# Performance work log

Hardware: AMD Instinct MI355X
Metric: run time of the kernel (lower is better)

The kernel has to match this reference:

```python
import jax, jax.numpy as jnp
import numpy as np

N = 100000      # nodes
E = 1600000     # edges
F_IN = 512      # num_features
H = 128         # hidden
C = 40          # num_classes
K = 10          # Chebyshev order


def setup_inputs() -> dict:
    key = jax.random.key(0)
    ks = jax.random.split(key, 6)
    x = jax.random.normal(ks[0], (N, F_IN), dtype=jnp.float32)
    edge_index = jax.random.randint(ks[1], (2, E), 0, N, dtype=jnp.int32)
    W1 = jax.random.normal(ks[2], (F_IN, H), dtype=jnp.float32) / np.sqrt(F_IN).astype(np.float32)
    b1 = jnp.zeros((H,), dtype=jnp.float32)
    W2 = jax.random.normal(ks[3], (H, C), dtype=jnp.float32) / np.sqrt(H).astype(np.float32)
    b2 = jnp.zeros((C,), dtype=jnp.float32)
    # Chebyshev coefficients temp[K+1]
    temp = 1.0 + 0.1 * jax.random.normal(ks[4], (K + 1,), dtype=jnp.float32)
    return {"x": x, "edge_index": edge_index, "W1": W1, "b1": b1, "W2": W2, "b2": b2, "temp": temp}


def reference(x, edge_index, W1, b1, W2, b2, temp):
    # MLP encoder (eval mode: dropout is identity)
    h = jax.nn.relu(x @ W1 + b1)          # [N, H]
    h = h @ W2 + b2                        # [N, C]

    # gcn_norm: add self-loops, symmetric normalization
    self_loop = jnp.arange(N, dtype=edge_index.dtype)
    row = jnp.concatenate([edge_index[0], self_loop])   # [E+N]
    col = jnp.concatenate([edge_index[1], self_loop])
    deg = jax.ops.segment_sum(jnp.ones_like(row, dtype=jnp.float32), row, num_segments=N)
    dis = jnp.where(deg > 0, jax.lax.rsqrt(jnp.maximum(deg, 1.0)), 0.0)
    norm = dis[row] * dis[col]             # [E+N]

    def prop(v):  # A_hat @ v : gather-scale-scatter over edges
        return jax.ops.segment_sum(norm[:, None] * v[col], row, num_segments=N)

    # Chebyshev recurrence: Tx_k = 2*A_hat*Tx_{k-1} - Tx_{k-2}
    Tx0 = h
    Tx1 = prop(h)
    out0 = temp[0] * Tx0 + temp[1] * Tx1

    def body(carry, coe):
        t0, t1, acc = carry
        t2 = 2.0 * prop(t1) - t0
        return (t1, t2, acc + coe * t2), None

    (_, _, out), _ = jax.lax.scan(body, (Tx0, Tx1, out0), temp[2:])
    return jax.nn.log_softmax(out, axis=1)
```

## Files before the change

### kernel.cpp

```cpp
#include <hip/hip_runtime.h>
#include <hip/hip_bf16.h>
#include <cstdint>
#include <cstddef>

#define NN   100000
#define EE   1600000
#define FIN  512
#define HID  128
#define CC   40
#define KORD 10
#define SHB  80
#define SHSTRIDE ((size_t)NN * SHB)

typedef __attribute__((ext_vector_type(4))) float f4;
typedef __attribute__((ext_vector_type(8))) short short8_t;
typedef __attribute__((ext_vector_type(4))) unsigned int u4;

__device__ __forceinline__ unsigned short cvt_bf16(float f) {
  union { float f; unsigned u; } a; a.f = f;
  unsigned r = a.u + 0x7fffu + ((a.u >> 16) & 1u);
  return (unsigned short)(r >> 16);
}
__device__ __forceinline__ unsigned pk_bf(float a, float b) {
  union { float f; unsigned u; } x, y; x.f = a; y.f = b;
  unsigned ra = x.u + 0x7fffu + ((x.u >> 16) & 1u);
  unsigned rb = y.u + 0x7fffu + ((y.u >> 16) & 1u);
  return (ra >> 16) | (rb & 0xffff0000u);
}
__device__ __forceinline__ unsigned pk_tr(float a, float b) {
  union { float f; unsigned u; } x, y; x.f = a; y.f = b;
  return (x.u >> 16) | (y.u & 0xffff0000u);
}
__device__ __forceinline__ f4 cvf2(unsigned lo, unsigned hi) {
  union { unsigned u; float f; } a, b, c, d;
  a.u = lo << 16; b.u = lo & 0xffff0000u;
  c.u = hi << 16; d.u = hi & 0xffff0000u;
  f4 r; r.x = a.f; r.y = b.f; r.z = c.f; r.w = d.f; return r;
}

__global__ __launch_bounds__(256) void k_dw(const int* __restrict__ rowI, int* __restrict__ deg,
                                            const float* __restrict__ W1, unsigned short* __restrict__ W1T,
                                            int ndeg) {
  int b = blockIdx.x;
  if (b < ndeg) {
    int i = b * 256 + threadIdx.x;
    if (i < EE) atomicAdd(&deg[rowI[i]], 1);
  } else {
    int idx = (b - ndeg) * 256 + threadIdx.x;
    int k = idx >> 7, n = idx & 127;
    W1T[(k >> 5) * 4096 + n * 32 + (k & 31)] = cvt_bf16(W1[idx]);
  }
}

__global__ __launch_bounds__(256) void k_scan1(const int* __restrict__ cnt, int* __restrict__ excl,
                                               int* __restrict__ bsums) {
  __shared__ int s[256];
  int tid = threadIdx.x;
  int base = blockIdx.x * 1024 + tid * 4;
  int v0 = (base + 0 < NN) ? cnt[base + 0] + 1 : 0;
  int v1 = (base + 1 < NN) ? cnt[base + 1] + 1 : 0;
  int v2 = (base + 2 < NN) ? cnt[base + 2] + 1 : 0;
  int v3 = (base + 3 < NN) ? cnt[base + 3] + 1 : 0;
  int tsum = v0 + v1 + v2 + v3;
  s[tid] = tsum;
  __syncthreads();
  for (int off = 1; off < 256; off <<= 1) {
    int t = (tid >= off) ? s[tid - off] : 0;
    __syncthreads();
    if (tid >= off) s[tid] += t;
    __syncthreads();
  }
  int run = s[tid] - tsum;
  if (tid == 255) bsums[blockIdx.x] = s[255];
  if (base + 0 < NN) excl[base + 0] = run; run += v0;
  if (base + 1 < NN) excl[base + 1] = run; run += v1;
  if (base + 2 < NN) excl[base + 2] = run; run += v2;
  if (base + 3 < NN) excl[base + 3] = run;
}

__global__ __launch_bounds__(128) void k_scan2(int* __restrict__ bsums, int nb) {
  __shared__ int s[128];
  int tid = threadIdx.x;
  int v = (tid < nb) ? bsums[tid] : 0;
  s[tid] = v;
  __syncthreads();
  for (int off = 1; off < 128; off <<= 1) {
    int t = (tid >= off) ? s[tid - off] : 0;
    __syncthreads();
    if (tid >= off) s[tid] += t;
    __syncthreads();
  }
  if (tid < nb) bsums[tid] = s[tid] - v;
}

__global__ __launch_bounds__(256) void k_scan3(const int* __restrict__ cnt, int* __restrict__ rs,
                                               int* __restrict__ cur, const int* __restrict__ bsums,
                                               float* __restrict__ dis, float* __restrict__ sqd,
                                               float* __restrict__ invd) {
  int i = blockIdx.x * 256 + threadIdx.x;
  if (i < NN) {
    int v = rs[i] + bsums[i >> 10];
    rs[i] = v;
    cur[i] = v;
    int d = cnt[i] + 1;
    if (i == NN - 1) rs[NN] = v + d;
    float fd = (float)d;
    dis[i]  = rsqrtf(fd);
    sqd[i]  = sqrtf(fd);
    invd[i] = 1.0f / fd;
  }
}

#define SLICE_ROWS (NN / 8)
#define SC_CHUNK   2048
__global__ __launch_bounds__(256) void k_scatter(const int* __restrict__ rowI, const int* __restrict__ colI,
                                                 int* __restrict__ cur, int* __restrict__ colS) {
  int slice = blockIdx.x & 7;
  int chunk = blockIdx.x >> 3;
  int lo = slice * SLICE_ROWS, hi = lo + SLICE_ROWS;
#pragma unroll
  for (int t = 0; t < SC_CHUNK / 256; ++t) {
    int i = chunk * SC_CHUNK + t * 256 + threadIdx.x;
    if (i < EE + NN) {
      int r = (i < EE) ? rowI[i] : (i - EE);
      if (r >= lo && r < hi) {
        int c = (i < EE) ? colI[i] : r;
        int pos = atomicAdd(&cur[r], 1);
        colS[pos] = c * SHB;
      }
    }
  }
}

#define LDK 40
__global__ __launch_bounds__(256) void k_gemm1(const float* __restrict__ x, const unsigned short* __restrict__ W1T,
                                               const float* __restrict__ b1, float* __restrict__ h1) {
  __shared__ __align__(16) float As_f[128 * 32];
  __shared__ __align__(16) short Bs_s[128][LDK];
  int tid  = threadIdx.x;
  int wave = tid >> 6, lane = tid & 63;
  int blockRow = blockIdx.x * 128;
  int wr = (wave & 1) * 64, wc = (wave >> 1) * 64;
  int l15 = lane & 15, hi4 = lane >> 4;

  int sr = (wave << 5) + (lane >> 3);
  int sslot = lane & 7;

  f4 acc[4][4] = {};

  for (int k0 = 0; k0 < FIN; k0 += 32) {
#pragma unroll
    for (int c = 0; c < 4; ++c) {
      int row = sr + c * 8;
      int gr = blockRow + row;
      int lslot = sslot ^ (row & 7);
      const float* gp = x + (size_t)gr * FIN + k0 + lslot * 4;
      float* lp = &As_f[(wave << 10) + (c << 8)];
      if (gr < NN) {
        __builtin_amdgcn_global_load_lds(
            (const __attribute__((address_space(1))) unsigned int*)gp,
            (__attribute__((address_space(3))) unsigned int*)lp, 16, 0, 0);
      }
    }

    const unsigned short* Wt = W1T + (k0 >> 5) * 4096;
    short8_t q0 = *(const short8_t*)&Wt[tid * 16];
    short8_t q1 = *(const short8_t*)&Wt[tid * 16 + 8];
    int bn = tid >> 1, bkk = (tid & 1) * 16;
    *(short8_t*)&Bs_s[bn][bkk]     = q0;
    *(short8_t*)&Bs_s[bn][bkk + 8] = q1;

    __syncthreads();

    short8_t afr[4], bfr[4];
#pragma unroll
    for (int m = 0; m < 4; ++m) {
      int row = wr + m * 16 + l15;
      int s0 = (hi4 * 2) ^ (row & 7);
      int s1 = (hi4 * 2 + 1) ^ (row & 7);
      f4 a0 = *(const f4*)&As_f[(row << 5) + s0 * 4];
      f4 a1 = *(const f4*)&As_f[(row << 5) + s1 * 4];
      u4 p;
      p.x = pk_tr(a0.x, a0.y); p.y = pk_tr(a0.z, a0.w);
      p.z = pk_tr(a1.x, a1.y); p.w = pk_tr(a1.z, a1.w);
      afr[m] = *(short8_t*)&p;
    }
#pragma unroll
    for (int n = 0; n < 4; ++n) bfr[n] = *(const short8_t*)&Bs_s[wc + n * 16 + l15][hi4 * 8];
#pragma unroll
    for (int m = 0; m < 4; ++m)
#pragma unroll
      for (int n = 0; n < 4; ++n)
        acc[m][n] = __builtin_amdgcn_mfma_f32_16x16x32_bf16(afr[m], bfr[n], acc[m][n], 0, 0, 0);

    __syncthreads();
  }

  float bias[4];
#pragma unroll
  for (int n = 0; n < 4; ++n) bias[n] = b1[wc + n * 16 + l15];
#pragma unroll
  for (int m = 0; m < 4; ++m) {
    int baseRow = blockRow + wr + m * 16 + hi4 * 4;
#pragma unroll
    for (int n = 0; n < 4; ++n) {
      int col = wc + n * 16 + l15;
#pragma unroll
      for (int r = 0; r < 4; ++r) {
        int grow = baseRow + r;
        if (grow < NN) h1[(size_t)grow * HID + col] = fmaxf(acc[m][n][r] + bias[n], 0.f);
      }
    }
  }
}

__global__ __launch_bounds__(256) void k_gemm2(const float* __restrict__ h1, const float* __restrict__ W2,
                                               const float* __restrict__ b2, const float* __restrict__ temp,
                                               const float* __restrict__ dis,
                                               unsigned short* __restrict__ sh0) {
  __shared__ float sW[HID * CC];
  __shared__ float sb[CC];
  int tid = threadIdx.x;
  for (int i = tid; i < HID * CC; i += 256) sW[i] = W2[i];
  if (tid < CC) sb[tid] = b2[tid];
  __syncthreads();
  int gid = blockIdx.x * 256 + tid;
  if (gid >= NN * 20) return;
  int row = gid / 20;
  int c2  = (gid - row * 20) * 2;
  const float* hr = h1 + (size_t)row * HID;
  float a0 = sb[c2], a1 = sb[c2 + 1];
#pragma unroll 8
  for (int k = 0; k < HID; ++k) {
    float hv = hr[k];
    a0 = fmaf(hv, sW[k * CC + c2], a0);
    a1 = fmaf(hv, sW[k * CC + c2 + 1], a1);
  }
  float dv = dis[row];
  *(unsigned*)((char*)sh0 + (size_t)row * SHB + c2 * 2) = pk_bf(a0 * dv, a1 * dv);
}

template <int MODE>
__global__ __launch_bounds__(256) void k_prop(const unsigned short* __restrict__ shIn,
                                              const unsigned short* __restrict__ shPrev,
                                              unsigned short* __restrict__ shOut,
                                              const int* __restrict__ colS,
                                              const int* __restrict__ rs,
                                              const float* __restrict__ invd) {
  int lane = threadIdx.x & 63;
  int wave = threadIdx.x >> 6;
  int grp  = lane / 5;
  int fi   = lane - grp * 5;
  int node = blockIdx.x * 48 + wave * 12 + grp;
  bool active = (grp < 12) && (node < NN);
  int s = 0, e = 0;
  if (active) { s = rs[node]; e = rs[node + 1]; }
  const char* base = (const char*)shIn + fi * 16;
  f4 lo0 = {0.f,0.f,0.f,0.f}, hi0 = lo0, lo1 = lo0, hi1 = lo0;
  f4 lo2 = lo0, hi2 = lo0, lo3 = lo0, hi3 = lo0;
  int j = s;
  for (; j + 8 <= e; j += 8) {
    int c0 = colS[j],     c1 = colS[j + 1], c2 = colS[j + 2], c3 = colS[j + 3];
    int c4 = colS[j + 4], c5 = colS[j + 5], c6 = colS[j + 6], c7 = colS[j + 7];
    u4 p0 = *(const u4*)(base + c0);
    u4 p1 = *(const u4*)(base + c1);
    u4 p2 = *(const u4*)(base + c2);
    u4 p3 = *(const u4*)(base + c3);
    u4 p4 = *(const u4*)(base + c4);
    u4 p5 = *(const u4*)(base + c5);
    u4 p6 = *(const u4*)(base + c6);
    u4 p7 = *(const u4*)(base + c7);
    lo0 += cvf2(p0.x, p0.y); hi0 += cvf2(p0.z, p0.w);
    lo1 += cvf2(p1.x, p1.y); hi1 += cvf2(p1.z, p1.w);
    lo2 += cvf2(p2.x, p2.y); hi2 += cvf2(p2.z, p2.w);
    lo3 += cvf2(p3.x, p3.y); hi3 += cvf2(p3.z, p3.w);
    lo0 += cvf2(p4.x, p4.y); hi0 += cvf2(p4.z, p4.w);
    lo1 += cvf2(p5.x, p5.y); hi1 += cvf2(p5.z, p5.w);
    lo2 += cvf2(p6.x, p6.y); hi2 += cvf2(p6.z, p6.w);
    lo3 += cvf2(p7.x, p7.y); hi3 += cvf2(p7.z, p7.w);
  }
  if (j + 4 <= e) {
    int c0 = colS[j], c1 = colS[j + 1], c2 = colS[j + 2], c3 = colS[j + 3];
    u4 p0 = *(const u4*)(base + c0);
    u4 p1 = *(const u4*)(base + c1);
    u4 p2 = *(const u4*)(base + c2);
    u4 p3 = *(const u4*)(base + c3);
    lo0 += cvf2(p0.x, p0.y); hi0 += cvf2(p0.z, p0.w);
    lo1 += cvf2(p1.x, p1.y); hi1 += cvf2(p1.z, p1.w);
    lo2 += cvf2(p2.x, p2.y); hi2 += cvf2(p2.z, p2.w);
    lo3 += cvf2(p3.x, p3.y); hi3 += cvf2(p3.z, p3.w);
    j += 4;
  }
  if (j + 2 <= e) {
    u4 p0 = *(const u4*)(base + colS[j]);
    u4 p1 = *(const u4*)(base + colS[j + 1]);
    lo0 += cvf2(p0.x, p0.y); hi0 += cvf2(p0.z, p0.w);
    lo1 += cvf2(p1.x, p1.y); hi1 += cvf2(p1.z, p1.w);
    j += 2;
  }
  if (j < e) {
    u4 p0 = *(const u4*)(base + colS[j]);
    lo2 += cvf2(p0.x, p0.y); hi2 += cvf2(p0.z, p0.w);
  }

  if (active) {
    f4 slo = (lo0 + lo1) + (lo2 + lo3);
    f4 shi = (hi0 + hi1) + (hi2 + hi3);
    float iv = invd[node];
    size_t ro = (size_t)node * SHB + fi * 16;
    f4 wlo, whi;
    if (MODE == 0) {
      wlo = iv * slo; whi = iv * shi;
    } else {
      u4 pp = *(const u4*)((const char*)shPrev + ro);
      f4 plo = cvf2(pp.x, pp.y), phi = cvf2(pp.z, pp.w);
      wlo = (2.f * iv) * slo - plo;
      whi = (2.f * iv) * shi - phi;
    }
    u4 pk;
    pk.x = pk_bf(wlo.x, wlo.y); pk.y = pk_bf(wlo.z, wlo.w);
    pk.z = pk_bf(whi.x, whi.y); pk.w = pk_bf(whi.z, whi.w);
    *(u4*)((char*)shOut + ro) = pk;
  }
}

__global__ __launch_bounds__(256) void k_comb(const unsigned short* __restrict__ shBase,
                                              float* __restrict__ outF,
                                              const float* __restrict__ sqd,
                                              const float* __restrict__ temp) {
  int lane = threadIdx.x & 63;
  int wave = threadIdx.x >> 6;
  int grp  = lane / 5;
  int fi   = lane - grp * 5;
  int node = blockIdx.x * 48 + wave * 12 + grp;
  if (grp >= 12 || node >= NN) return;

  const char* p = (const char*)shBase + (size_t)node * SHB + fi * 16;
  f4 alo = {0.f,0.f,0.f,0.f}, ahi = alo;
#pragma unroll
  for (int k = 0; k <= KORD; ++k) {
    u4 pp = *(const u4*)(p + (size_t)k * SHSTRIDE);
    float tk = temp[k];
    alo += tk * cvf2(pp.x, pp.y);
    ahi += tk * cvf2(pp.z, pp.w);
  }
  float sq = sqd[node];
  alo *= sq; ahi *= sq;

  int gb = grp * 5;
  float m = fmaxf(fmaxf(fmaxf(alo.x, alo.y), fmaxf(alo.z, alo.w)),
                  fmaxf(fmaxf(ahi.x, ahi.y), fmaxf(ahi.z, ahi.w)));
  float mm = m;
#pragma unroll
  for (int j = 0; j < 5; ++j) mm = fmaxf(mm, __shfl(m, gb + j));
  float ss = expf(alo.x - mm) + expf(alo.y - mm) + expf(alo.z - mm) + expf(alo.w - mm)
           + expf(ahi.x - mm) + expf(ahi.y - mm) + expf(ahi.z - mm) + expf(ahi.w - mm);
  float tot = 0.f;
#pragma unroll
  for (int j = 0; j < 5; ++j) tot += __shfl(ss, gb + j);
  float lse = mm + logf(tot);
  alo -= lse; ahi -= lse;
  size_t o = (size_t)node * CC + fi * 8;
  *(f4*)&outF[o]     = alo;
  *(f4*)&outF[o + 4] = ahi;
}

extern "C" void kernel_launch(void* const* d_in, const int* in_sizes, int n_in,
                              void* d_out, int out_size, void* d_ws, size_t ws_size,
                              hipStream_t stream) {
  const float* x    = (const float*)d_in[0];
  const int*   ei   = (const int*)d_in[1];
  const float* W1   = (const float*)d_in[2];
  const float* b1   = (const float*)d_in[3];
  const float* W2   = (const float*)d_in[4];
  const float* b2   = (const float*)d_in[5];
  const float* temp = (const float*)d_in[6];
  const int* rowI = ei;
  const int* colI = ei + EE;
  float* out = (float*)d_out;

  char* w = (char*)d_ws;
  auto alloc = [&](size_t bytes) -> void* {
    void* p = (void*)w;
    w += (bytes + 255) & ~(size_t)255;
    return p;
  };
  int*   deg   = (int*)  alloc((size_t)NN * 4);
  float* dis   = (float*)alloc((size_t)NN * 4);
  float* sqd   = (float*)alloc((size_t)NN * 4);
  float* invd  = (float*)alloc((size_t)NN * 4);
  int*   rs    = (int*)  alloc((size_t)(NN + 1) * 4);
  int*   cur   = (int*)  alloc((size_t)NN * 4);
  int*   bsums = (int*)  alloc(512 * 4);
  unsigned short* W1T = (unsigned short*)alloc((size_t)FIN * HID * 2);
  unsigned short* shAll = (unsigned short*)alloc(SHSTRIDE * (KORD + 1));
  int*   colS  = (int*)  alloc((size_t)(EE + NN) * 4);
  float* h1    = (float*)alloc((size_t)NN * HID * 4);

  auto sh = [&](int k) -> unsigned short* {
    return (unsigned short*)((char*)shAll + (size_t)k * SHSTRIDE);
  };

  hipMemsetAsync(deg, 0, (size_t)NN * 4, stream);

  const int NDEG = (EE + 255) / 256;
  const int NW1T = FIN * HID / 256;
  k_dw<<<NDEG + NW1T, 256, 0, stream>>>(rowI, deg, W1, W1T, NDEG);

  int nb = (NN + 1023) / 1024;
  k_scan1<<<nb, 256, 0, stream>>>(deg, rs, bsums);
  k_scan2<<<1, 128, 0, stream>>>(bsums, nb);
  k_scan3<<<(NN + 255) / 256, 256, 0, stream>>>(deg, rs, cur, bsums, dis, sqd, invd);

  const int NCH = (EE + NN + SC_CHUNK - 1) / SC_CHUNK;
  k_scatter<<<8 * NCH, 256, 0, stream>>>(rowI, colI, cur, colS);

  k_gemm1<<<(NN + 127) / 128, 256, 0, stream>>>(x, W1T, b1, h1);
  k_gemm2<<<(NN * 20 + 255) / 256, 256, 0, stream>>>(h1, W2, b2, temp, dis, sh(0));

  int G = (NN + 47) / 48;
  k_prop<0><<<G, 256, 0, stream>>>(sh(0), sh(0), sh(1), colS, rs, invd);
  for (int k = 2; k <= KORD; ++k) {
    k_prop<1><<<G, 256, 0, stream>>>(sh(k - 1), sh(k - 2), sh(k), colS, rs, invd);
  }

  k_comb<<<G, 256, 0, stream>>>(shAll, out, sqd, temp);
}
```

Baseline: 625.8 us.

## Split feature layout into column blocks and propagate block-wise with XCC-aware chunk scheduling

Each Chebyshev term is stored as three separate column blocks (features 0-15, 16-31, 32-39) instead of 80-byte interleaved rows. Each propagation kernel processes one block per workgroup, and workgroups claim chunks through atomic cursors whose starting block depends on the XCC ID. The aim is to shrink the gathered working set per pass so it fits in the per-XCC L2 cache, and to use vectorized colS loads. In exchange it adds atomic work distribution, more index loads per edge (colS is read once per block pass), and a dependence on the hardware XCC register.

```diff
diff --git a/kernel.cpp b/kernel.cpp
--- a/kernel.cpp
+++ b/kernel.cpp
@@ -9,12 +9,18 @@
 #define HID  128
 #define CC   40
 #define KORD 10
-#define SHB  80
-#define SHSTRIDE ((size_t)NN * SHB)
+#define SHSTRIDE ((size_t)NN * 80)
+#define BLKB ((size_t)NN * 32)
+#define BLKC ((size_t)NN * 64)
+#define CHA 782
+#define CHB 782
+#define CHC 391
+#define PGRID 2048
 
 typedef __attribute__((ext_vector_type(4))) float f4;
 typedef __attribute__((ext_vector_type(8))) short short8_t;
 typedef __attribute__((ext_vector_type(4))) unsigned int u4;
+typedef __attribute__((ext_vector_type(4), aligned(4))) int i4u;
 
 __device__ __forceinline__ unsigned short cvt_bf16(float f) {
   union { float f; unsigned u; } a; a.f = f;
@@ -126,7 +132,7 @@
       if (r >= lo && r < hi) {
         int c = (i < EE) ? colI[i] : r;
         int pos = atomicAdd(&cur[r], 1);
-        colS[pos] = c * SHB;
+        colS[pos] = c * 32;
       }
     }
   }
@@ -212,6 +218,12 @@
       }
     }
   }
+}
+
+__device__ __forceinline__ size_t sh_off(int node, int fi) {
+  return (fi < 2) ? ((size_t)node * 32 + fi * 16)
+       : (fi < 4) ? (BLKB + (size_t)node * 32 + (fi - 2) * 16)
+                  : (BLKC + (size_t)node * 16);
 }
 
 __global__ __launch_bounds__(256) void k_gemm2(const float* __restrict__ h1, const float* __restrict__ W2,
@@ -237,90 +249,182 @@
     a1 = fmaf(hv, sW[k * CC + c2 + 1], a1);
   }
   float dv = dis[row];
-  *(unsigned*)((char*)sh0 + (size_t)row * SHB + c2 * 2) = pk_bf(a0 * dv, a1 * dv);
+  size_t ro;
+  if (c2 < 16)      ro = (size_t)row * 32 + c2 * 2;
+  else if (c2 < 32) ro = BLKB + (size_t)row * 32 + (c2 - 16) * 2;
+  else              ro = BLKC + (size_t)row * 16 + (c2 - 32) * 2;
+  *(unsigned*)((char*)sh0 + ro) = pk_bf(a0 * dv, a1 * dv);
 }
 
 template <int MODE>
-__global__ __launch_bounds__(256) void k_prop(const unsigned short* __restrict__ shIn,
-                                              const unsigned short* __restrict__ shPrev,
-                                              unsigned short* __restrict__ shOut,
-                                              const int* __restrict__ colS,
-                                              const int* __restrict__ rs,
-                                              const float* __restrict__ invd) {
-  int lane = threadIdx.x & 63;
-  int wave = threadIdx.x >> 6;
-  int grp  = lane / 5;
-  int fi   = lane - grp * 5;
-  int node = blockIdx.x * 48 + wave * 12 + grp;
-  bool active = (grp < 12) && (node < NN);
-  int s = 0, e = 0;
-  if (active) { s = rs[node]; e = rs[node + 1]; }
-  const char* base = (const char*)shIn + fi * 16;
-  f4 lo0 = {0.f,0.f,0.f,0.f}, hi0 = lo0, lo1 = lo0, hi1 = lo0;
-  f4 lo2 = lo0, hi2 = lo0, lo3 = lo0, hi3 = lo0;
-  int j = s;
-  for (; j + 8 <= e; j += 8) {
-    int c0 = colS[j],     c1 = colS[j + 1], c2 = colS[j + 2], c3 = colS[j + 3];
-    int c4 = colS[j + 4], c5 = colS[j + 5], c6 = colS[j + 6], c7 = colS[j + 7];
-    u4 p0 = *(const u4*)(base + c0);
-    u4 p1 = *(const u4*)(base + c1);
-    u4 p2 = *(const u4*)(base + c2);
-    u4 p3 = *(const u4*)(base + c3);
-    u4 p4 = *(const u4*)(base + c4);
-    u4 p5 = *(const u4*)(base + c5);
-    u4 p6 = *(const u4*)(base + c6);
-    u4 p7 = *(const u4*)(base + c7);
-    lo0 += cvf2(p0.x, p0.y); hi0 += cvf2(p0.z, p0.w);
-    lo1 += cvf2(p1.x, p1.y); hi1 += cvf2(p1.z, p1.w);
-    lo2 += cvf2(p2.x, p2.y); hi2 += cvf2(p2.z, p2.w);
-    lo3 += cvf2(p3.x, p3.y); hi3 += cvf2(p3.z, p3.w);
-    lo0 += cvf2(p4.x, p4.y); hi0 += cvf2(p4.z, p4.w);
-    lo1 += cvf2(p5.x, p5.y); hi1 += cvf2(p5.z, p5.w);
-    lo2 += cvf2(p6.x, p6.y); hi2 += cvf2(p6.z, p6.w);
-    lo3 += cvf2(p7.x, p7.y); hi3 += cvf2(p7.z, p7.w);
-  }
-  if (j + 4 <= e) {
-    int c0 = colS[j], c1 = colS[j + 1], c2 = colS[j + 2], c3 = colS[j + 3];
-    u4 p0 = *(const u4*)(base + c0);
-    u4 p1 = *(const u4*)(base + c1);
-    u4 p2 = *(const u4*)(base + c2);
-    u4 p3 = *(const u4*)(base + c3);
-    lo0 += cvf2(p0.x, p0.y); hi0 += cvf2(p0.z, p0.w);
-    lo1 += cvf2(p1.x, p1.y); hi1 += cvf2(p1.z, p1.w);
-    lo2 += cvf2(p2.x, p2.y); hi2 += cvf2(p2.z, p2.w);
-    lo3 += cvf2(p3.x, p3.y); hi3 += cvf2(p3.z, p3.w);
-    j += 4;
-  }
-  if (j + 2 <= e) {
-    u4 p0 = *(const u4*)(base + colS[j]);
-    u4 p1 = *(const u4*)(base + colS[j + 1]);
-    lo0 += cvf2(p0.x, p0.y); hi0 += cvf2(p0.z, p0.w);
-    lo1 += cvf2(p1.x, p1.y); hi1 += cvf2(p1.z, p1.w);
-    j += 2;
-  }
-  if (j < e) {
-    u4 p0 = *(const u4*)(base + colS[j]);
-    lo2 += cvf2(p0.x, p0.y); hi2 += cvf2(p0.z, p0.w);
-  }
-
-  if (active) {
-    f4 slo = (lo0 + lo1) + (lo2 + lo3);
-    f4 shi = (hi0 + hi1) + (hi2 + hi3);
-    float iv = invd[node];
-    size_t ro = (size_t)node * SHB + fi * 16;
-    f4 wlo, whi;
-    if (MODE == 0) {
-      wlo = iv * slo; whi = iv * shi;
-    } else {
-      u4 pp = *(const u4*)((const char*)shPrev + ro);
-      f4 plo = cvf2(pp.x, pp.y), phi = cvf2(pp.z, pp.w);
-      wlo = (2.f * iv) * slo - plo;
-      whi = (2.f * iv) * shi - phi;
-    }
-    u4 pk;
-    pk.x = pk_bf(wlo.x, wlo.y); pk.y = pk_bf(wlo.z, wlo.w);
-    pk.z = pk_bf(whi.x, whi.y); pk.w = pk_bf(whi.z, whi.w);
-    *(u4*)((char*)shOut + ro) = pk;
+__global__ __launch_bounds__(256) void k_prop3(const unsigned short* __restrict__ shIn,
+                                               const unsigned short* __restrict__ shPrev,
+                                               unsigned short* __restrict__ shOut,
+                                               const int* __restrict__ colS,
+                                               const int* __restrict__ rs,
+                                               const float* __restrict__ invd,
+                                               int* __restrict__ cursors) {
+  __shared__ int s_pass, s_chunk;
+  if (threadIdx.x == 0) {
+    unsigned xcc;
+    asm volatile("s_getreg_b32 %0, hwreg(HW_REG_XCC_ID, 0, 32)" : "=s"(xcc));
+    int x = (int)(xcc & 7);
+    int pref = (x < 3) ? 0 : (x < 6) ? 1 : 2;
+    int pass = -1, chunk = -1;
+    for (int t = 0; t < 3; ++t) {
+      int p = pref + t; if (p >= 3) p -= 3;
+      int lim = (p == 0) ? CHA : (p == 1) ? CHB : CHC;
+      int c = atomicAdd(&cursors[p], 1);
+      if (c < lim) { pass = p; chunk = c; break; }
+    }
+    s_pass = pass; s_chunk = chunk;
+  }
+  __syncthreads();
+  int pass = s_pass;
+  if (pass < 0) return;
+  int chunk = s_chunk;
+  int lane = threadIdx.x & 63, wave = threadIdx.x >> 6;
+
+  if (pass < 2) {
+    size_t pb = (pass == 0) ? (size_t)0 : BLKB;
+    int grp = lane >> 1, fi = lane & 1;
+    int node = chunk * 128 + wave * 32 + grp;
+    bool act = node < NN;
+    int s = 0, e = 0;
+    if (act) { s = rs[node]; e = rs[node + 1]; }
+    const char* base = (const char*)shIn + pb + fi * 16;
+    f4 a0 = {0.f,0.f,0.f,0.f}, b0 = a0, a1 = a0, b1 = a0;
+    int j = s;
+    for (; j + 8 <= e; j += 8) {
+      i4u ca = *(const i4u*)&colS[j];
+      i4u cb = *(const i4u*)&colS[j + 4];
+      u4 p0 = *(const u4*)(base + ca.x);
+      u4 p1 = *(const u4*)(base + ca.y);
+      u4 p2 = *(const u4*)(base + ca.z);
+      u4 p3 = *(const u4*)(base + ca.w);
+      u4 p4 = *(const u4*)(base + cb.x);
+      u4 p5 = *(const u4*)(base + cb.y);
+      u4 p6 = *(const u4*)(base + cb.z);
+      u4 p7 = *(const u4*)(base + cb.w);
+      a0 += cvf2(p0.x, p0.y); b0 += cvf2(p0.z, p0.w);
+      a1 += cvf2(p1.x, p1.y); b1 += cvf2(p1.z, p1.w);
+      a0 += cvf2(p2.x, p2.y); b0 += cvf2(p2.z, p2.w);
+      a1 += cvf2(p3.x, p3.y); b1 += cvf2(p3.z, p3.w);
+      a0 += cvf2(p4.x, p4.y); b0 += cvf2(p4.z, p4.w);
+      a1 += cvf2(p5.x, p5.y); b1 += cvf2(p5.z, p5.w);
+      a0 += cvf2(p6.x, p6.y); b0 += cvf2(p6.z, p6.w);
+      a1 += cvf2(p7.x, p7.y); b1 += cvf2(p7.z, p7.w);
+    }
+    if (j + 4 <= e) {
+      i4u ca = *(const i4u*)&colS[j];
+      u4 p0 = *(const u4*)(base + ca.x);
+      u4 p1 = *(const u4*)(base + ca.y);
+      u4 p2 = *(const u4*)(base + ca.z);
+      u4 p3 = *(const u4*)(base + ca.w);
+      a0 += cvf2(p0.x, p0.y); b0 += cvf2(p0.z, p0.w);
+      a1 += cvf2(p1.x, p1.y); b1 += cvf2(p1.z, p1.w);
+      a0 += cvf2(p2.x, p2.y); b0 += cvf2(p2.z, p2.w);
+      a1 += cvf2(p3.x, p3.y); b1 += cvf2(p3.z, p3.w);
+      j += 4;
+    }
+    if (j + 2 <= e) {
+      u4 p0 = *(const u4*)(base + colS[j]);
+      u4 p1 = *(const u4*)(base + colS[j + 1]);
+      a0 += cvf2(p0.x, p0.y); b0 += cvf2(p0.z, p0.w);
+      a1 += cvf2(p1.x, p1.y); b1 += cvf2(p1.z, p1.w);
+      j += 2;
+    }
+    if (j < e) {
+      u4 p0 = *(const u4*)(base + colS[j]);
+      a0 += cvf2(p0.x, p0.y); b0 += cvf2(p0.z, p0.w);
+    }
+    if (act) {
+      f4 slo = a0 + a1, shi = b0 + b1;
+      float iv = invd[node];
+      size_t ro = pb + (size_t)node * 32 + fi * 16;
+      f4 wlo, whi;
+      if (MODE == 0) {
+        wlo = iv * slo; whi = iv * shi;
+      } else {
+        u4 pp = __builtin_nontemporal_load((const u4*)((const char*)shPrev + ro));
+        f4 plo = cvf2(pp.x, pp.y), phi = cvf2(pp.z, pp.w);
+        wlo = (2.f * iv) * slo - plo;
+        whi = (2.f * iv) * shi - phi;
+      }
+      u4 pk;
+      pk.x = pk_bf(wlo.x, wlo.y); pk.y = pk_bf(wlo.z, wlo.w);
+      pk.z = pk_bf(whi.x, whi.y); pk.w = pk_bf(whi.z, whi.w);
+      *(u4*)((char*)shOut + ro) = pk;
+    }
+  } else {
+    int node = chunk * 256 + wave * 64 + lane;
+    bool act = node < NN;
+    int s = 0, e = 0;
+    if (act) { s = rs[node]; e = rs[node + 1]; }
+    const char* base = (const char*)shIn + BLKC;
+    f4 a0 = {0.f,0.f,0.f,0.f}, b0 = a0, a1 = a0, b1 = a0;
+    int j = s;
+    for (; j + 8 <= e; j += 8) {
+      i4u ca = *(const i4u*)&colS[j];
+      i4u cb = *(const i4u*)&colS[j + 4];
+      u4 p0 = *(const u4*)(base + (ca.x >> 1));
+      u4 p1 = *(const u4*)(base + (ca.y >> 1));
+      u4 p2 = *(const u4*)(base + (ca.z >> 1));
+      u4 p3 = *(const u4*)(base + (ca.w >> 1));
+      u4 p4 = *(const u4*)(base + (cb.x >> 1));
+      u4 p5 = *(const u4*)(base + (cb.y >> 1));
+      u4 p6 = *(const u4*)(base + (cb.z >> 1));
+      u4 p7 = *(const u4*)(base + (cb.w >> 1));
+      a0 += cvf2(p0.x, p0.y); b0 += cvf2(p0.z, p0.w);
+      a1 += cvf2(p1.x, p1.y); b1 += cvf2(p1.z, p1.w);
+      a0 += cvf2(p2.x, p2.y); b0 += cvf2(p2.z, p2.w);
+      a1 += cvf2(p3.x, p3.y); b1 += cvf2(p3.z, p3.w);
+      a0 += cvf2(p4.x, p4.y); b0 += cvf2(p4.z, p4.w);
+      a1 += cvf2(p5.x, p5.y); b1 += cvf2(p5.z, p5.w);
+      a0 += cvf2(p6.x, p6.y); b0 += cvf2(p6.z, p6.w);
+      a1 += cvf2(p7.x, p7.y); b1 += cvf2(p7.z, p7.w);
+    }
+    if (j + 4 <= e) {
+      i4u ca = *(const i4u*)&colS[j];
+      u4 p0 = *(const u4*)(base + (ca.x >> 1));
+      u4 p1 = *(const u4*)(base + (ca.y >> 1));
+      u4 p2 = *(const u4*)(base + (ca.z >> 1));
+      u4 p3 = *(const u4*)(base + (ca.w >> 1));
+      a0 += cvf2(p0.x, p0.y); b0 += cvf2(p0.z, p0.w);
+      a1 += cvf2(p1.x, p1.y); b1 += cvf2(p1.z, p1.w);
+      a0 += cvf2(p2.x, p2.y); b0 += cvf2(p2.z, p2.w);
+      a1 += cvf2(p3.x, p3.y); b1 += cvf2(p3.z, p3.w);
+      j += 4;
+    }
+    if (j + 2 <= e) {
+      u4 p0 = *(const u4*)(base + (colS[j] >> 1));
+      u4 p1 = *(const u4*)(base + (colS[j + 1] >> 1));
+      a0 += cvf2(p0.x, p0.y); b0 += cvf2(p0.z, p0.w);
+      a1 += cvf2(p1.x, p1.y); b1 += cvf2(p1.z, p1.w);
+      j += 2;
+    }
+    if (j < e) {
+      u4 p0 = *(const u4*)(base + (colS[j] >> 1));
+      a0 += cvf2(p0.x, p0.y); b0 += cvf2(p0.z, p0.w);
+    }
+    if (act) {
+      f4 slo = a0 + a1, shi = b0 + b1;
+      float iv = invd[node];
+      size_t ro = BLKC + (size_t)node * 16;
+      f4 wlo, whi;
+      if (MODE == 0) {
+        wlo = iv * slo; whi = iv * shi;
+      } else {
+        u4 pp = __builtin_nontemporal_load((const u4*)((const char*)shPrev + ro));
+        f4 plo = cvf2(pp.x, pp.y), phi = cvf2(pp.z, pp.w);
+        wlo = (2.f * iv) * slo - plo;
+        whi = (2.f * iv) * shi - phi;
+      }
+      u4 pk;
+      pk.x = pk_bf(wlo.x, wlo.y); pk.y = pk_bf(wlo.z, wlo.w);
+      pk.z = pk_bf(whi.x, whi.y); pk.w = pk_bf(whi.z, whi.w);
+      *(u4*)((char*)shOut + ro) = pk;
+    }
   }
 }
 
@@ -335,7 +439,7 @@
   int node = blockIdx.x * 48 + wave * 12 + grp;
   if (grp >= 12 || node >= NN) return;
 
-  const char* p = (const char*)shBase + (size_t)node * SHB + fi * 16;
+  const char* p = (const char*)shBase + sh_off(node, fi);
   f4 alo = {0.f,0.f,0.f,0.f}, ahi = alo;
 #pragma unroll
   for (int k = 0; k <= KORD; ++k) {
@@ -392,6 +496,7 @@
   int*   rs    = (int*)  alloc((size_t)(NN + 1) * 4);
   int*   cur   = (int*)  alloc((size_t)NN * 4);
   int*   bsums = (int*)  alloc(512 * 4);
+  int*   curs  = (int*)  alloc(16 * 4 * 4);
   unsigned short* W1T = (unsigned short*)alloc((size_t)FIN * HID * 2);
   unsigned short* shAll = (unsigned short*)alloc(SHSTRIDE * (KORD + 1));
   int*   colS  = (int*)  alloc((size_t)(EE + NN) * 4);
@@ -402,6 +507,7 @@
   };
 
   hipMemsetAsync(deg, 0, (size_t)NN * 4, stream);
+  hipMemsetAsync(curs, 0, 16 * 4 * 4, stream);
 
   const int NDEG = (EE + 255) / 256;
   const int NW1T = FIN * HID / 256;
@@ -418,11 +524,10 @@
   k_gemm1<<<(NN + 127) / 128, 256, 0, stream>>>(x, W1T, b1, h1);
   k_gemm2<<<(NN * 20 + 255) / 256, 256, 0, stream>>>(h1, W2, b2, temp, dis, sh(0));
 
-  int G = (NN + 47) / 48;
-  k_prop<0><<<G, 256, 0, stream>>>(sh(0), sh(0), sh(1), colS, rs, invd);
+  k_prop3<0><<<PGRID, 256, 0, stream>>>(sh(0), sh(0), sh(1), colS, rs, invd, curs);
   for (int k = 2; k <= KORD; ++k) {
-    k_prop<1><<<G, 256, 0, stream>>>(sh(k - 1), sh(k - 2), sh(k), colS, rs, invd);
-  }
-
-  k_comb<<<G, 256, 0, stream>>>(shAll, out, sqd, temp);
-}
+    k_prop3<1><<<PGRID, 256, 0, stream>>>(sh(k - 1), sh(k - 2), sh(k), colS, rs, invd, curs + (k - 1) * 4);
+  }
+
+  k_comb<<<(NN + 47) / 48, 256, 0, stream>>>(shAll, out, sqd, temp);
+}
```

Result: slower. 817.1 us (+30.6%).
